# Kernel optimization log

Hardware: AMD Instinct MI355X
Metric: run time of the kernel (lower is better)

The kernel has to match this reference:

```python
import jax, jax.numpy as jnp
import numpy as np


def setup_inputs() -> dict:
    key = jax.random.key(0)
    k1, k2, k3 = jax.random.split(key, 3)
    B, T, F = 32, 8192, 80
    ODIM, IDIM = 1024, 640
    src_tokens = jax.random.normal(k1, (B, T, F), dtype=jnp.float32)
    src_lengths = jax.random.randint(k2, (B,), 3, T + 1, dtype=jnp.int64)
    # xavier_normal_ on Linear weight [odim, idim]
    std = float(np.sqrt(2.0 / (ODIM + IDIM)))
    W = jax.random.normal(k3, (ODIM, IDIM), dtype=jnp.float32) * std
    b = jnp.zeros((ODIM,), dtype=jnp.float32)
    return {"src_tokens": src_tokens, "src_lengths": src_lengths, "W": W, "b": b}


def reference(src_tokens, src_lengths, W, b):
    B, T, F = src_tokens.shape
    n_frames = (T // 3) * 3
    out_lengths = src_lengths // 3 - 2
    # stack 3 consecutive frames: cat(x[:, ::3], x[:, 1::3], x[:, 2::3], -1) == reshape
    x = src_tokens[:, :n_frames, :].reshape(B, n_frames // 3, 3 * F)  # [B, M, 240]
    # window of 3 stacked frames -> feature 9F = 720, then keep first 640
    x = jnp.concatenate((x[:, :-2, :], x[:, 1:-1, :], x[:, 2:, :]), axis=-1)  # [B, M-2, 720]
    x = x[:, :, : x.shape[-1] - 80]  # [B, M-2, 640]
    x = jnp.transpose(x, (1, 0, 2))  # [T', B, 640]
    y = jnp.einsum("tbi,oi->tbo", x, W) + b  # [T', B, odim]
    # GLU on dim=1 (the batch dim, as in the original code)
    half = y.shape[1] // 2
    x_out = y[:, :half, :] * jax.nn.sigmoid(y[:, half:, :])  # [T', B/2, odim]
    return (x_out, out_lengths)
```

## Files before the change

### kernel.cpp

```cpp
#include <hip/hip_runtime.h>

#define GLOBAL_AS __attribute__((address_space(1)))
#define LDS_AS    __attribute__((address_space(3)))

typedef __bf16 bf16x8 __attribute__((ext_vector_type(8)));
typedef float  f32x4  __attribute__((ext_vector_type(4)));

constexpr int SRC_STRIDE = 8192 * 80;
constexpr int TOUT       = 2728;
constexpr long OUT_ELEMS = (long)TOUT * 16 * 1024;
constexpr int SRC_ELEMS  = 32 * SRC_STRIDE;
constexpr int W_ELEMS    = 1024 * 640;
constexpr int MBLK       = 341;
constexpr int NT         = 20;
constexpr int SLOT       = 16384;

__device__ __forceinline__ unsigned short f2bf(float f) {
    union { float f; unsigned u; } a; a.f = f;
    unsigned r = a.u + 0x7FFF + ((a.u >> 16) & 1);
    return (unsigned short)(r >> 16);
}

__global__ void cvt_kernel(const float* __restrict__ in, unsigned short* __restrict__ out, int n4) {
    int i = blockIdx.x * blockDim.x + threadIdx.x;
    if (i >= n4) return;
    float4 v = ((const float4*)in)[i];
    ushort4 o;
    o.x = f2bf(v.x); o.y = f2bf(v.y); o.z = f2bf(v.z); o.w = f2bf(v.w);
    ((ushort4*)out)[i] = o;
}

__global__ void lengths_kernel(const int* __restrict__ len, float* __restrict__ out) {
    int i = threadIdx.x;
    if (i < 32) out[OUT_ELEMS + i] = (float)(len[i] / 3 - 2);
}

#define MFMA_ROW(a_, i_)                                                         \
    acc[i_][0] = __builtin_amdgcn_mfma_f32_16x16x32_bf16(a_, bv0, acc[i_][0],0,0,0); \
    acc[i_][1] = __builtin_amdgcn_mfma_f32_16x16x32_bf16(a_, bv1, acc[i_][1],0,0,0); \
    acc[i_][2] = __builtin_amdgcn_mfma_f32_16x16x32_bf16(a_, bv2, acc[i_][2],0,0,0); \
    acc[i_][3] = __builtin_amdgcn_mfma_f32_16x16x32_bf16(a_, bv3, acc[i_][3],0,0,0);

__global__ __launch_bounds__(512, 2)
void glu_gemm(const __bf16* __restrict__ A,
              const __bf16* __restrict__ Wb,
              const float* __restrict__ bias,
              float* __restrict__ out) {
    __shared__ __bf16 lds[4 * SLOT];

    const int tid  = threadIdx.x;
    const int lane = tid & 63;
    const int w    = tid >> 6;
    const int wm   = w >> 2;
    const int wn   = w & 3;

    const int bid = blockIdx.x;
    const int bn  = (bid >> 3) & 3;
    const int bm  = (bid >> 5) * 8 + (bid & 7);
    if (bm >= MBLK) return;

    const int sl  = lane >> 3;
    const int sp  = lane & 7;
    const int sc  = sp ^ sl;
    const int scc = (sc & 3) * 8;
    const int srp = sc >> 2;
    int aG[2], bG[2];
#pragma unroll
    for (int h = 0; h < 2; ++h) {
        int R = 2 * (h * 64 + w * 8 + sl) + srp;
        int m = bm * 256 + R;
        aG[h] = (m & 31) * SRC_STRIDE + (m >> 5) * 240 + scc;
        int n = bn * 256 + R;
        bG[h] = n * 640 + scc;
    }
    const int aD0 = (w * 8) * 64;
    const int aD1 = (64 + w * 8) * 64;
    const int bD0 = 8192 + aD0;
    const int bD1 = 8192 + aD1;

    const int ll  = (lane & 15) >> 1;
    const int pfr = (((lane & 1) << 2) | (lane >> 4)) ^ ll;
    const int aB  = (wm * 64 + ll) * 64 + pfr * 8;
    const int bB  = 8192 + (wn * 32 + ll) * 64 + pfr * 8;

    const unsigned LB    = (unsigned)(unsigned long long)(&lds[0]);
    const unsigned adrA0 = LB + 2u * (unsigned)aB;
    const unsigned adrB0 = LB + 2u * (unsigned)bB;

    f32x4 acc[8][4] = {};

#pragma unroll
    for (int t = 0; t < 3; ++t) {
        const int so = t * SLOT;
        const int kg = t * 32;
        __builtin_amdgcn_global_load_lds((const GLOBAL_AS void*)(A + (aG[0] + kg)),
                                         (LDS_AS void*)(lds + so + aD0), 16, 0, 0);
        __builtin_amdgcn_global_load_lds((const GLOBAL_AS void*)(A + (aG[1] + kg)),
                                         (LDS_AS void*)(lds + so + aD1), 16, 0, 0);
        __builtin_amdgcn_global_load_lds((const GLOBAL_AS void*)(Wb + (bG[0] + kg)),
                                         (LDS_AS void*)(lds + so + bD0), 16, 0, 0);
        __builtin_amdgcn_global_load_lds((const GLOBAL_AS void*)(Wb + (bG[1] + kg)),
                                         (LDS_AS void*)(lds + so + bD1), 16, 0, 0);
    }
    asm volatile("s_waitcnt vmcnt(8)" ::: "memory");
    __builtin_amdgcn_s_barrier();

    for (int t = 0; t < NT; ++t) {
        const unsigned so16 = (unsigned)(t & 3) << 15;
        const unsigned aAdr = adrA0 + so16;
        const unsigned bAdr = adrB0 + so16;
        const int nxt = ((t + 3) & 3) * SLOT;
        const int kg  = (t + 3) * 32;
        const bool st = (t < NT - 3);

        bf16x8 af0, af1, af2, af3, bv0, bv1, bv2, bv3;
        asm volatile("ds_read_b128 %0, %1 offset:0"    : "=v"(af0) : "v"(aAdr));
        asm volatile("ds_read_b128 %0, %1 offset:1024" : "=v"(af1) : "v"(aAdr));
        asm volatile("ds_read_b128 %0, %1 offset:2048" : "=v"(af2) : "v"(aAdr));
        asm volatile("ds_read_b128 %0, %1 offset:3072" : "=v"(af3) : "v"(aAdr));
        asm volatile("ds_read_b128 %0, %1 offset:0"    : "=v"(bv0) : "v"(bAdr));
        asm volatile("ds_read_b128 %0, %1 offset:1024" : "=v"(bv1) : "v"(bAdr));
        asm volatile("ds_read_b128 %0, %1 offset:2048" : "=v"(bv2) : "v"(bAdr));
        asm volatile("ds_read_b128 %0, %1 offset:3072" : "=v"(bv3) : "v"(bAdr));
        if (st) {
            __builtin_amdgcn_global_load_lds((const GLOBAL_AS void*)(A + (aG[0] + kg)),
                                             (LDS_AS void*)(lds + nxt + aD0), 16, 0, 0);
            __builtin_amdgcn_global_load_lds((const GLOBAL_AS void*)(A + (aG[1] + kg)),
                                             (LDS_AS void*)(lds + nxt + aD1), 16, 0, 0);
        }
        __builtin_amdgcn_s_barrier();
        asm volatile("s_waitcnt lgkmcnt(0)" ::: "memory");
        __builtin_amdgcn_sched_barrier(0);
        __builtin_amdgcn_s_setprio(1);
        MFMA_ROW(af0, 0) MFMA_ROW(af1, 1) MFMA_ROW(af2, 2) MFMA_ROW(af3, 3)
        __builtin_amdgcn_s_setprio(0);
        __builtin_amdgcn_s_barrier();

        bf16x8 ag0, ag1, ag2, ag3;
        asm volatile("ds_read_b128 %0, %1 offset:4096" : "=v"(ag0) : "v"(aAdr));
        asm volatile("ds_read_b128 %0, %1 offset:5120" : "=v"(ag1) : "v"(aAdr));
        asm volatile("ds_read_b128 %0, %1 offset:6144" : "=v"(ag2) : "v"(aAdr));
        asm volatile("ds_read_b128 %0, %1 offset:7168" : "=v"(ag3) : "v"(aAdr));
        if (st) {
            __builtin_amdgcn_global_load_lds((const GLOBAL_AS void*)(Wb + (bG[0] + kg)),
                                             (LDS_AS void*)(lds + nxt + bD0), 16, 0, 0);
            __builtin_amdgcn_global_load_lds((const GLOBAL_AS void*)(Wb + (bG[1] + kg)),
                                             (LDS_AS void*)(lds + nxt + bD1), 16, 0, 0);
        }
        __builtin_amdgcn_s_barrier();
        asm volatile("s_waitcnt lgkmcnt(0)" ::: "memory");
        __builtin_amdgcn_sched_barrier(0);
        __builtin_amdgcn_s_setprio(1);
        MFMA_ROW(ag0, 4) MFMA_ROW(ag1, 5) MFMA_ROW(ag2, 6) MFMA_ROW(ag3, 7)
        __builtin_amdgcn_s_setprio(0);

        if (t < NT - 3)       asm volatile("s_waitcnt vmcnt(8)" ::: "memory");
        else if (t == NT - 3) asm volatile("s_waitcnt vmcnt(4)" ::: "memory");
        else if (t == NT - 2) asm volatile("s_waitcnt vmcnt(0)" ::: "memory");
        __builtin_amdgcn_s_barrier();
    }

    const int col = lane & 15;
    const int q   = lane >> 4;
    float bvs[4];
#pragma unroll
    for (int nf = 0; nf < 4; ++nf)
        bvs[nf] = bias[bn * 256 + wn * 64 + nf * 16 + col];

    const int tb = bm * 8 + wm * 4;
#pragma unroll
    for (int i = 0; i < 4; ++i) {
        const int t = tb + i;
#pragma unroll
        for (int nf = 0; nf < 4; ++nf) {
            const int n = bn * 256 + wn * 64 + nf * 16 + col;
#pragma unroll
            for (int r2 = 0; r2 < 4; ++r2) {
                const int brow = q * 4 + r2;
                float v = acc[2 * i][nf][r2] + bvs[nf];
                float g = acc[2 * i + 1][nf][r2] + bvs[nf];
                float s = 1.0f / (1.0f + __expf(-g));
                out[((long)(t * 16 + brow)) * 1024 + n] = v * s;
            }
        }
    }
}

extern "C" void kernel_launch(void* const* d_in, const int* in_sizes, int n_in,
                              void* d_out, int out_size, void* d_ws, size_t ws_size,
                              hipStream_t stream) {
    const float* src  = (const float*)d_in[0];
    const int*   lens = (const int*)d_in[1];
    const float* Wf   = (const float*)d_in[2];
    const float* bias = (const float*)d_in[3];
    float* out = (float*)d_out;

    unsigned short* srcb = (unsigned short*)d_ws;
    unsigned short* wb   = srcb + SRC_ELEMS;

    cvt_kernel<<<SRC_ELEMS / 4 / 256, 256, 0, stream>>>(src, srcb, SRC_ELEMS / 4);
    cvt_kernel<<<W_ELEMS / 4 / 256, 256, 0, stream>>>(Wf, wb, W_ELEMS / 4);

    lengths_kernel<<<1, 64, 0, stream>>>(lens, out);

    glu_gemm<<<43 * 32, 512, 0, stream>>>((const __bf16*)srcb, (const __bf16*)wb, bias, out);
}
```

Measured before the change: 362.2 us.

## Double-buffer LDS fragments in registers and cut barriers per K-tile

Restructures the GEMM main loop to prefetch the next K-tile's A and B fragments from LDS into a second register set (even/odd ping-pong) while MFMAs run on the current set. This removes the LDS-read-to-MFMA stall and drops the barriers per tile from three to one. Global-to-LDS staging is issued at the top of each tile with a relaxed vmcnt wait. The cost is higher register pressure from 24 live fragment vectors, which could cause spills at 2 blocks per CU, and a more fragile synchronisation scheme.

```diff
diff --git a/kernel.cpp b/kernel.cpp
--- a/kernel.cpp
+++ b/kernel.cpp
@@ -12,7 +12,6 @@
 constexpr int SRC_ELEMS  = 32 * SRC_STRIDE;
 constexpr int W_ELEMS    = 1024 * 640;
 constexpr int MBLK       = 341;
-constexpr int NT         = 20;
 constexpr int SLOT       = 16384;
 
 __device__ __forceinline__ unsigned short f2bf(float f) {
@@ -35,11 +34,59 @@
     if (i < 32) out[OUT_ELEMS + i] = (float)(len[i] / 3 - 2);
 }
 
-#define MFMA_ROW(a_, i_)                                                         \
-    acc[i_][0] = __builtin_amdgcn_mfma_f32_16x16x32_bf16(a_, bv0, acc[i_][0],0,0,0); \
-    acc[i_][1] = __builtin_amdgcn_mfma_f32_16x16x32_bf16(a_, bv1, acc[i_][1],0,0,0); \
-    acc[i_][2] = __builtin_amdgcn_mfma_f32_16x16x32_bf16(a_, bv2, acc[i_][2],0,0,0); \
-    acc[i_][3] = __builtin_amdgcn_mfma_f32_16x16x32_bf16(a_, bv3, acc[i_][3],0,0,0);
+#define GLD(gp, lp) __builtin_amdgcn_global_load_lds((const GLOBAL_AS void*)(gp), \
+                                                     (LDS_AS void*)(lp), 16, 0, 0)
+
+#define STAGE_T(tile_) do {                                    \
+    const int kg_ = (tile_) * 32;                              \
+    const int so_ = ((tile_) & 3) * SLOT;                      \
+    GLD(A  + (aG[0] + kg_), lds + so_ + aD0);                  \
+    GLD(A  + (aG[1] + kg_), lds + so_ + aD1);                  \
+    GLD(Wb + (bG[0] + kg_), lds + so_ + bD0);                  \
+    GLD(Wb + (bG[1] + kg_), lds + so_ + bD1);                  \
+} while (0)
+
+#define READ_B4_A4(P, sa_, sb_)                                                  \
+    asm volatile("ds_read_b128 %0, %1 offset:0"    : "=v"(b##P##0) : "v"(sb_));  \
+    asm volatile("ds_read_b128 %0, %1 offset:1024" : "=v"(b##P##1) : "v"(sb_));  \
+    asm volatile("ds_read_b128 %0, %1 offset:2048" : "=v"(b##P##2) : "v"(sb_));  \
+    asm volatile("ds_read_b128 %0, %1 offset:3072" : "=v"(b##P##3) : "v"(sb_));  \
+    asm volatile("ds_read_b128 %0, %1 offset:0"    : "=v"(a##P##0) : "v"(sa_));  \
+    asm volatile("ds_read_b128 %0, %1 offset:1024" : "=v"(a##P##1) : "v"(sa_));  \
+    asm volatile("ds_read_b128 %0, %1 offset:2048" : "=v"(a##P##2) : "v"(sa_));  \
+    asm volatile("ds_read_b128 %0, %1 offset:3072" : "=v"(a##P##3) : "v"(sa_));
+
+#define READ_A4HI(P, sa_)                                                        \
+    asm volatile("ds_read_b128 %0, %1 offset:4096" : "=v"(a##P##4) : "v"(sa_));  \
+    asm volatile("ds_read_b128 %0, %1 offset:5120" : "=v"(a##P##5) : "v"(sa_));  \
+    asm volatile("ds_read_b128 %0, %1 offset:6144" : "=v"(a##P##6) : "v"(sa_));  \
+    asm volatile("ds_read_b128 %0, %1 offset:7168" : "=v"(a##P##7) : "v"(sa_));
+
+#define MR4(a_, P, i_)                                                                  \
+    acc[i_][0] = __builtin_amdgcn_mfma_f32_16x16x32_bf16(a_, b##P##0, acc[i_][0],0,0,0); \
+    acc[i_][1] = __builtin_amdgcn_mfma_f32_16x16x32_bf16(a_, b##P##1, acc[i_][1],0,0,0); \
+    acc[i_][2] = __builtin_amdgcn_mfma_f32_16x16x32_bf16(a_, b##P##2, acc[i_][2],0,0,0); \
+    acc[i_][3] = __builtin_amdgcn_mfma_f32_16x16x32_bf16(a_, b##P##3, acc[i_][3],0,0,0);
+
+#define MFMA_LO(P) MR4(a##P##0, P, 0) MR4(a##P##1, P, 1) MR4(a##P##2, P, 2) MR4(a##P##3, P, 3)
+#define MFMA_HI(P) MR4(a##P##4, P, 4) MR4(a##P##5, P, 5) MR4(a##P##6, P, 6) MR4(a##P##7, P, 7)
+
+#define TILE(CUR, NXT, t_, do_stage_) do {                                       \
+    if (do_stage_) STAGE_T((t_) + 3);                                            \
+    const unsigned soff_ = (unsigned)((((t_) + 1) & 3) << 15);                   \
+    const unsigned sa_ = adrA0 + soff_;                                          \
+    const unsigned sb_ = adrB0 + soff_;                                          \
+    READ_B4_A4(NXT, sa_, sb_)                                                    \
+    asm volatile("s_waitcnt lgkmcnt(8)" ::: "memory");                           \
+    __builtin_amdgcn_sched_barrier(0);                                           \
+    __builtin_amdgcn_s_setprio(1);                                               \
+    MFMA_LO(CUR)                                                                 \
+    __builtin_amdgcn_s_setprio(0);                                               \
+    READ_A4HI(NXT, sa_)                                                          \
+    __builtin_amdgcn_s_setprio(1);                                               \
+    MFMA_HI(CUR)                                                                 \
+    __builtin_amdgcn_s_setprio(0);                                               \
+} while (0)
 
 __global__ __launch_bounds__(512, 2)
 void glu_gemm(const __bf16* __restrict__ A,
@@ -88,77 +135,40 @@
     const unsigned adrB0 = LB + 2u * (unsigned)bB;
 
     f32x4 acc[8][4] = {};
-
-#pragma unroll
-    for (int t = 0; t < 3; ++t) {
-        const int so = t * SLOT;
-        const int kg = t * 32;
-        __builtin_amdgcn_global_load_lds((const GLOBAL_AS void*)(A + (aG[0] + kg)),
-                                         (LDS_AS void*)(lds + so + aD0), 16, 0, 0);
-        __builtin_amdgcn_global_load_lds((const GLOBAL_AS void*)(A + (aG[1] + kg)),
-                                         (LDS_AS void*)(lds + so + aD1), 16, 0, 0);
-        __builtin_amdgcn_global_load_lds((const GLOBAL_AS void*)(Wb + (bG[0] + kg)),
-                                         (LDS_AS void*)(lds + so + bD0), 16, 0, 0);
-        __builtin_amdgcn_global_load_lds((const GLOBAL_AS void*)(Wb + (bG[1] + kg)),
-                                         (LDS_AS void*)(lds + so + bD1), 16, 0, 0);
-    }
-    asm volatile("s_waitcnt vmcnt(8)" ::: "memory");
+    bf16x8 aE0, aE1, aE2, aE3, aE4, aE5, aE6, aE7, bE0, bE1, bE2, bE3;
+    bf16x8 aO0, aO1, aO2, aO3, aO4, aO5, aO6, aO7, bO0, bO1, bO2, bO3;
+
+    STAGE_T(0); STAGE_T(1); STAGE_T(2);
+    asm volatile("s_waitcnt vmcnt(4)" ::: "memory");
     __builtin_amdgcn_s_barrier();
-
-    for (int t = 0; t < NT; ++t) {
-        const unsigned so16 = (unsigned)(t & 3) << 15;
-        const unsigned aAdr = adrA0 + so16;
-        const unsigned bAdr = adrB0 + so16;
-        const int nxt = ((t + 3) & 3) * SLOT;
-        const int kg  = (t + 3) * 32;
-        const bool st = (t < NT - 3);
-
-        bf16x8 af0, af1, af2, af3, bv0, bv1, bv2, bv3;
-        asm volatile("ds_read_b128 %0, %1 offset:0"    : "=v"(af0) : "v"(aAdr));
-        asm volatile("ds_read_b128 %0, %1 offset:1024" : "=v"(af1) : "v"(aAdr));
-        asm volatile("ds_read_b128 %0, %1 offset:2048" : "=v"(af2) : "v"(aAdr));
-        asm volatile("ds_read_b128 %0, %1 offset:3072" : "=v"(af3) : "v"(aAdr));
-        asm volatile("ds_read_b128 %0, %1 offset:0"    : "=v"(bv0) : "v"(bAdr));
-        asm volatile("ds_read_b128 %0, %1 offset:1024" : "=v"(bv1) : "v"(bAdr));
-        asm volatile("ds_read_b128 %0, %1 offset:2048" : "=v"(bv2) : "v"(bAdr));
-        asm volatile("ds_read_b128 %0, %1 offset:3072" : "=v"(bv3) : "v"(bAdr));
-        if (st) {
-            __builtin_amdgcn_global_load_lds((const GLOBAL_AS void*)(A + (aG[0] + kg)),
-                                             (LDS_AS void*)(lds + nxt + aD0), 16, 0, 0);
-            __builtin_amdgcn_global_load_lds((const GLOBAL_AS void*)(A + (aG[1] + kg)),
-                                             (LDS_AS void*)(lds + nxt + aD1), 16, 0, 0);
-        }
+    __builtin_amdgcn_sched_barrier(0);
+    {
+        const unsigned sa_ = adrA0;
+        const unsigned sb_ = adrB0;
+        READ_B4_A4(E, sa_, sb_)
+        READ_A4HI(E, sa_)
+    }
+
+#pragma unroll 1
+    for (int i = 0; i < 9; ++i) {
+        const int t = 2 * i;
+        TILE(E, O, t, 1);
+        asm volatile("s_waitcnt vmcnt(4)" ::: "memory");
         __builtin_amdgcn_s_barrier();
-        asm volatile("s_waitcnt lgkmcnt(0)" ::: "memory");
         __builtin_amdgcn_sched_barrier(0);
-        __builtin_amdgcn_s_setprio(1);
-        MFMA_ROW(af0, 0) MFMA_ROW(af1, 1) MFMA_ROW(af2, 2) MFMA_ROW(af3, 3)
-        __builtin_amdgcn_s_setprio(0);
+        TILE(O, E, t + 1, (i < 8));
+        if (i < 8) asm volatile("s_waitcnt vmcnt(4)" ::: "memory");
+        else       asm volatile("s_waitcnt vmcnt(0)" ::: "memory");
         __builtin_amdgcn_s_barrier();
-
-        bf16x8 ag0, ag1, ag2, ag3;
-        asm volatile("ds_read_b128 %0, %1 offset:4096" : "=v"(ag0) : "v"(aAdr));
-        asm volatile("ds_read_b128 %0, %1 offset:5120" : "=v"(ag1) : "v"(aAdr));
-        asm volatile("ds_read_b128 %0, %1 offset:6144" : "=v"(ag2) : "v"(aAdr));
-        asm volatile("ds_read_b128 %0, %1 offset:7168" : "=v"(ag3) : "v"(aAdr));
-        if (st) {
-            __builtin_amdgcn_global_load_lds((const GLOBAL_AS void*)(Wb + (bG[0] + kg)),
-                                             (LDS_AS void*)(lds + nxt + bD0), 16, 0, 0);
-            __builtin_amdgcn_global_load_lds((const GLOBAL_AS void*)(Wb + (bG[1] + kg)),
-                                             (LDS_AS void*)(lds + nxt + bD1), 16, 0, 0);
-        }
-        __builtin_amdgcn_s_barrier();
-        asm volatile("s_waitcnt lgkmcnt(0)" ::: "memory");
         __builtin_amdgcn_sched_barrier(0);
-        __builtin_amdgcn_s_setprio(1);
-        MFMA_ROW(ag0, 4) MFMA_ROW(ag1, 5) MFMA_ROW(ag2, 6) MFMA_ROW(ag3, 7)
-        __builtin_amdgcn_s_setprio(0);
-
-        if (t < NT - 3)       asm volatile("s_waitcnt vmcnt(8)" ::: "memory");
-        else if (t == NT - 3) asm volatile("s_waitcnt vmcnt(4)" ::: "memory");
-        else if (t == NT - 2) asm volatile("s_waitcnt vmcnt(0)" ::: "memory");
-        __builtin_amdgcn_s_barrier();
-    }
+    }
+    TILE(E, O, 18, 0);
+    asm volatile("s_waitcnt lgkmcnt(0)" ::: "memory");
+    __builtin_amdgcn_sched_barrier(0);
+    __builtin_amdgcn_s_setprio(1);
+    MFMA_LO(O)
+    MFMA_HI(O)
+    __builtin_amdgcn_s_setprio(0);
 
     const int col = lane & 15;
     const int q   = lane >> 4;
```

New measurement: 368.1 us. Within noise of the previous version (+1.6%).
